# Performance work log

Hardware: AMD Instinct MI355X
Metric: run time of the kernel (lower is better)

The kernel has to match this reference:

```python
import jax, jax.numpy as jnp
import numpy as np

N = 4096      # num_nodes
U = 64        # num_units
IN = 2        # input_dim
DIM = U + IN  # 66
H = 4         # attention heads
ALPHA = 0.2   # leaky slope inside attention scores
SLOPE = 0.01  # nn.LeakyReLU() default for subnet activations
NEG_INF = -9e15


def setup_inputs() -> dict:
    key = jax.random.key(0)
    ks = jax.random.split(key, 20)
    def gn(k, shape, fan):
        return jax.random.normal(k, shape, dtype=jnp.float32) / np.float32(np.sqrt(fan))
    adj = jax.random.randint(ks[2], (N, N), 0, 2, dtype=jnp.int32)
    adj = jnp.maximum(adj, jnp.eye(N, dtype=jnp.int32))  # ensure self-loops
    return {
        "inputs": jax.random.normal(ks[0], (1, N * IN), dtype=jnp.float32),
        "hx": jax.random.normal(ks[1], (1, N, U), dtype=jnp.float32),
        "adj": adj,
        "m1_W": gn(ks[3], (H, DIM, DIM), DIM),
        "m1_a1": gn(ks[4], (H, DIM), DIM),
        "m1_a2": gn(ks[5], (H, DIM), DIM),
        "m1_Wout": gn(ks[6], (H * DIM, DIM), H * DIM),
        "m1_ao1": gn(ks[7], (DIM,), DIM),
        "m1_ao2": gn(ks[8], (DIM,), DIM),
        "m2_W": gn(ks[9], (H, DIM, DIM), DIM),
        "m2_a1": gn(ks[10], (H, DIM), DIM),
        "m2_a2": gn(ks[11], (H, DIM), DIM),
        "m2_Wout": gn(ks[12], (H * DIM, DIM), H * DIM),
        "m2_ao1": gn(ks[13], (DIM,), DIM),
        "m2_ao2": gn(ks[14], (DIM,), DIM),
        "g1_W": gn(ks[15], (DIM, 2 * U), DIM),
        "g1_b": jnp.zeros((2 * U,), dtype=jnp.float32),
        "g2_W": gn(ks[16], (DIM, U), DIM),
        "g2_b": jnp.zeros((U,), dtype=jnp.float32),
    }


def gat_layer(x, W, a1, a2, mask):
    # x: [N,Fin], W: [Fin,Fout], a1/a2: [Fout], mask: [N,N] bool
    h = x @ W                                   # [N,Fout]
    f1 = h @ a1                                 # [N] source term
    f2 = h @ a2                                 # [N] target term
    e = jax.nn.leaky_relu(f1[:, None] + f2[None, :], ALPHA)  # [N,N]
    e = jnp.where(mask, e, NEG_INF)
    attn = jax.nn.softmax(e, axis=-1)
    return attn @ h                             # [N,Fout]


def subnet(x, W, a1, a2, Wout, ao1, ao2, mask):
    # multi-head GAT, concat heads, activation, output GAT layer, activation
    heads = jax.vmap(gat_layer, in_axes=(None, 0, 0, 0, None))(x, W, a1, a2, mask)  # [H,N,DIM]
    hcat = jnp.transpose(heads, (1, 0, 2)).reshape(x.shape[0], -1)                   # [N,H*DIM]
    hcat = jax.nn.leaky_relu(hcat, SLOPE)
    out = gat_layer(hcat, Wout, ao1, ao2, mask)                                      # [N,DIM]
    return jax.nn.leaky_relu(out, SLOPE)


def reference(inputs, hx, adj, m1_W, m1_a1, m1_a2, m1_Wout, m1_ao1, m1_ao2,
              m2_W, m2_a1, m2_a2, m2_Wout, m2_ao1, m2_ao2,
              g1_W, g1_b, g2_W, g2_b):
    mask = adj > 0
    xi = inputs.reshape(N, IN)
    xh = hx.reshape(N, U)
    # _GAT1: concat(inputs, hx) -> GATSubNet1 -> linear -> sigmoid -> split r,u
    x1 = jnp.concatenate([xi, xh], axis=-1)                 # [N,DIM]
    g1 = subnet(x1, m1_W, m1_a1, m1_a2, m1_Wout, m1_ao1, m1_ao2, mask)
    value = jax.nn.sigmoid(g1 @ g1_W + g1_b)                # [N,2U]
    r, u = value[:, :U], value[:, U:]
    # _GAT2: concat(inputs, r*hx) -> GATSubNet2 -> linear -> tanh
    x2 = jnp.concatenate([xi, r * xh], axis=-1)             # [N,DIM]
    g2 = subnet(x2, m2_W, m2_a1, m2_a2, m2_Wout, m2_ao1, m2_ao2, mask)
    c = jnp.tanh(g2 @ g2_W + g2_b)                          # [N,U]
    new_state = u * xh + (1.0 - u) * c
    return new_state.reshape(1, N, U)
```

## Files before the change

### kernel.cpp

```cpp
#include <hip/hip_runtime.h>

constexpr int kN = 4096;
constexpr int kDim = 66;
constexpr int kU = 64;
constexpr float kAlpha = 0.2f;
constexpr float kSlope = 0.01f;
constexpr float kLog2e = 1.44269504f;

typedef _Float16 half8 __attribute__((ext_vector_type(8)));
typedef _Float16 half2t __attribute__((ext_vector_type(2)));
typedef float floatx4 __attribute__((ext_vector_type(4)));

__device__ inline unsigned int fkey(float f){
  unsigned int u = __float_as_uint(f);
  return (u & 0x80000000u) ? ~u : (u | 0x80000000u);
}
__device__ inline float funkey(unsigned int k){
  unsigned int u = (k & 0x80000000u) ? (k ^ 0x80000000u) : ~k;
  return __uint_as_float(u);
}

__global__ void setup_k(const int* __restrict__ adj, unsigned long long* __restrict__ packed,
                        const float* __restrict__ in2, const float* __restrict__ hx,
                        _Float16* __restrict__ x1b, _Float16* __restrict__ x2b,
                        const float* __restrict__ m1W, const float* __restrict__ m1a1, const float* __restrict__ m1a2,
                        const float* __restrict__ m1Wo, const float* __restrict__ m1ao1, const float* __restrict__ m1ao2,
                        const float* __restrict__ m2W, const float* __restrict__ m2a1, const float* __restrict__ m2a2,
                        const float* __restrict__ m2Wo, const float* __restrict__ m2ao1, const float* __restrict__ m2ao2,
                        const float* __restrict__ g1W, const float* __restrict__ g1b,
                        const float* __restrict__ g2W, const float* __restrict__ g2b,
                        _Float16* __restrict__ B1t, _Float16* __restrict__ B1t2,
                        _Float16* __restrict__ B2t, _Float16* __restrict__ B2t2,
                        _Float16* __restrict__ Bgt, _Float16* __restrict__ Bft,
                        unsigned int* __restrict__ fmaxbuf){
  int bb = blockIdx.x, t = threadIdx.x;
  if (bb < 16384){
    int gid = bb * 256 + t;
    unsigned long long m = __ballot(adj[gid] != 0);
    if ((t & 63) == 0) packed[gid >> 6] = m;
    return;
  }
  if (bb < 16384 + 1024){
    int i = (bb - 16384) * 4 + (t >> 6);
    int c = t & 63;
    x1b[(size_t)i * 96 + 2 + c] = (_Float16)hx[(size_t)i * kU + c];
    if (c < 2){
      _Float16 xv = (_Float16)in2[i * 2 + c];
      x1b[(size_t)i * 96 + c] = xv;
      x2b[(size_t)i * 96 + c] = xv;
    }
    if (c < 30){
      x1b[(size_t)i * 96 + 66 + c] = (_Float16)0.f;
      x2b[(size_t)i * 96 + 66 + c] = (_Float16)0.f;
    }
    return;
  }
  int b = bb - (16384 + 1024);
  if (b < 8){
    int m = b & 3;
    const float* W  = (b < 4 ? m1W  : m2W)  + (size_t)m * kDim * kDim;
    const float* a1 = (b < 4 ? m1a1 : m2a1) + m * kDim;
    const float* a2 = (b < 4 ? m1a2 : m2a2) + m * kDim;
    _Float16* Bo = (b < 4 ? B1t : B1t2) + (size_t)m * 80 * 96;
    __shared__ float Ws[kDim * kDim];
    __shared__ float wa1s[kDim], wa2s[kDim];
    for (int z = t; z < kDim * kDim; z += 256) Ws[z] = W[z];
    __syncthreads();
    if (t < kDim){
      float s1 = 0.f, s2 = 0.f;
      for (int d = 0; d < kDim; d++){ float wv = Ws[t * kDim + d]; s1 += wv * a1[d]; s2 += wv * a2[d]; }
      wa1s[t] = s1; wa2s[t] = s2;
    }
    __syncthreads();
    for (int z = t; z < 80 * 96; z += 256){
      int nn = z / 96, k = z % 96;
      float val = 0.f;
      if (k < kDim){
        if (nn < kDim) val = Ws[k * kDim + nn];
        else if (nn == 66) val = wa1s[k];
        else if (nn == 67) val = wa2s[k];
      }
      Bo[z] = (_Float16)val;
    }
  } else if (b < 10){
    const float* Wo  = (b == 8 ? m1Wo  : m2Wo);
    const float* ao1 = (b == 8 ? m1ao1 : m2ao1);
    const float* ao2 = (b == 8 ? m1ao2 : m2ao2);
    _Float16* Bo = (b == 8 ? B2t : B2t2);
    __shared__ float wo1s[264], wo2s[264];
    for (int k = t; k < 264; k += 256){
      float s1 = 0.f, s2 = 0.f;
      for (int d = 0; d < kDim; d++){ float wv = Wo[(size_t)k * kDim + d]; s1 += wv * ao1[d]; s2 += wv * ao2[d]; }
      wo1s[k] = s1; wo2s[k] = s2;
    }
    __syncthreads();
    for (int z = t; z < 80 * 288; z += 256){
      int nn = z / 288, k = z % 288;
      float val = 0.f;
      if (k < 264){
        if (nn < kDim) val = Wo[(size_t)k * kDim + nn];
        else if (nn == 66) val = wo1s[k];
        else if (nn == 67) val = wo2s[k];
      }
      Bo[z] = (_Float16)val;
    }
  } else if (b == 10){
    for (int z = t; z < 128 * 96; z += 256){
      int nn = z / 96, k = z % 96;
      float val = 0.f;
      if (k < kDim) val = g1W[k * 128 + nn];
      else if (k == 66) val = g1b[nn];
      Bgt[z] = (_Float16)val;
    }
  } else {
    if (t < 16) fmaxbuf[t] = 0u;
    for (int z = t; z < 64 * 96; z += 256){
      int nn = z / 96, k = z % 96;
      float val = 0.f;
      if (k < kDim) val = g2W[k * 64 + nn];
      else if (k == 66) val = g2b[nn];
      Bft[z] = (_Float16)val;
    }
  }
}

template<int KSTEPS, int NT>
__device__ __forceinline__ void gemmN(const _Float16* __restrict__ Arow,
                                      const _Float16* __restrict__ Bt, floatx4* acc){
  const int lane = threadIdx.x & 63, q = lane >> 4, n = lane & 15;
  #pragma unroll
  for (int v = 0; v < NT; v++) acc[v] = (floatx4){0.f, 0.f, 0.f, 0.f};
  #pragma unroll
  for (int ks = 0; ks < KSTEPS; ks++){
    half8 af = *(const half8*)&Arow[ks * 32 + q * 8];
    #pragma unroll
    for (int nt = 0; nt < NT; nt++){
      half8 bf = *(const half8*)&Bt[(size_t)(nt * 16 + n) * (KSTEPS * 32) + ks * 32 + q * 8];
      acc[nt] = __builtin_amdgcn_mfma_f32_16x16x32_f16(af, bf, acc[nt], 0, 0, 0);
    }
  }
}

__device__ __forceinline__ void epi0(floatx4* acc, int i0, _Float16* __restrict__ Htc,
                                     float* __restrict__ f1c, float* __restrict__ f2c,
                                     unsigned* __restrict__ fmaxslot){
  const int t = threadIdx.x, w = t >> 6, lane = t & 63, q = lane >> 4, n = lane & 15;
  const int ib = i0 + w * 16 + q * 4;
  float lm = -3e38f;
  #pragma unroll
  for (int nt = 0; nt < 5; nt++){
    int c = nt * 16 + n;
    if (c < kDim){
      union { _Float16 h[4]; uint2 v; } pk;
      pk.h[0] = (_Float16)acc[nt][0]; pk.h[1] = (_Float16)acc[nt][1];
      pk.h[2] = (_Float16)acc[nt][2]; pk.h[3] = (_Float16)acc[nt][3];
      *(uint2*)&Htc[(size_t)c * kN + ib] = pk.v;
    } else if (c == 66){
      float4 fv; fv.x = acc[nt][0] * kLog2e; fv.y = acc[nt][1] * kLog2e;
      fv.z = acc[nt][2] * kLog2e; fv.w = acc[nt][3] * kLog2e;
      *(float4*)&f1c[ib] = fv;
      *(uint2*)&Htc[(size_t)66 * kN + ib] = make_uint2(0x3C003C00u, 0x3C003C00u);
    } else if (c == 67){
      float4 fv; fv.x = acc[nt][0] * kLog2e; fv.y = acc[nt][1] * kLog2e;
      fv.z = acc[nt][2] * kLog2e; fv.w = acc[nt][3] * kLog2e;
      *(float4*)&f2c[ib] = fv;
      lm = fmaxf(fmaxf(fv.x, fv.y), fmaxf(fv.z, fv.w));
      *(uint2*)&Htc[(size_t)67 * kN + ib] = make_uint2(0u, 0u);
    }
  }
  lm = fmaxf(lm, __shfl_xor(lm, 16));
  lm = fmaxf(lm, __shfl_xor(lm, 32));
  if (lane == 3) atomicMax(fmaxslot, fkey(lm));
}

__global__ __launch_bounds__(256) void gemm_ht_k(
    const _Float16* __restrict__ A, const _Float16* __restrict__ Bt,
    _Float16* __restrict__ Ht, float* __restrict__ f1, float* __restrict__ f2,
    unsigned int* __restrict__ fmaxp)
{
  const int m = blockIdx.y;
  const int i0 = blockIdx.x * 64;
  const int w = threadIdx.x >> 6, n = threadIdx.x & 15;
  floatx4 acc[5];
  gemmN<3, 5>(A + (size_t)(i0 + w * 16 + n) * 96, Bt + (size_t)m * 80 * 96, acc);
  epi0(acc, i0, Ht + (size_t)m * 80 * kN, f1 + (size_t)m * kN, f2 + (size_t)m * kN, fmaxp + m);
}

template<int TPW, int KSR>
__global__ __launch_bounds__(256, 2) void attn_mfma_k(
    const _Float16* __restrict__ Ht, const float* __restrict__ f1,
    const float* __restrict__ f2, const unsigned int* __restrict__ fmaxu,
    const unsigned long long* __restrict__ packed,
    _Float16* __restrict__ paccb)
{
  constexpr int WJ = KSR * 32;
  const int m = blockIdx.y;
  const int t = threadIdx.x;
  const int w = t >> 6, lane = t & 63, q = lane >> 4, n = lane & 15;
  const int i0b = blockIdx.x * (TPW * 64);
  const int wrb = i0b + w * (TPW * 16);
  const int jbase = blockIdx.z * WJ;
  const _Float16* Hg = Ht + (size_t)m * 80 * kN;
  const float* f2m = f2 + (size_t)m * kN;
  const float* f1m = f1 + (size_t)m * kN;
  const float fmx = funkey(fmaxu[m]);

  __shared__ __align__(16) _Float16 B1h[WJ], B2h[WJ];
  for (int z = t; z < WJ; z += 256){
    float v = f2m[jbase + z] - fmx;
    B1h[z] = (_Float16)__builtin_amdgcn_exp2f(v);
    B2h[z] = (_Float16)__builtin_amdgcn_exp2f(kAlpha * v);
  }
  __syncthreads();

  half2t a1p[TPW], a2p[TPW];
  const unsigned long long* prow[TPW];
  #pragma unroll
  for (int a = 0; a < TPW; a++){
    int i = wrb + a * 16 + n;
    float t0 = f1m[i] + fmx;
    float S = fmaxf(t0, kAlpha * t0);
    _Float16 A1 = (_Float16)__builtin_amdgcn_exp2f(t0 - S);
    _Float16 A2 = (_Float16)__builtin_amdgcn_exp2f(kAlpha * t0 - S);
    a1p[a] = (half2t){A1, A1};
    a2p[a] = (half2t){A2, A2};
    prow[a] = packed + (size_t)i * 64;
  }

  floatx4 acc[TPW][5];
  #pragma unroll
  for (int a = 0; a < TPW; a++)
    #pragma unroll
    for (int v = 0; v < 5; v++) acc[a][v] = (floatx4){0.f, 0.f, 0.f, 0.f};

  unsigned long long mw[TPW];
  #pragma unroll
  for (int ks = 0; ks < KSR; ks++){
    if ((ks & 1) == 0){
      int widx = (jbase >> 6) + (ks >> 1);
      #pragma unroll
      for (int a = 0; a < TPW; a++) mw[a] = prow[a][widx];
    }
    const unsigned shift = (ks & 1) * 32 + q * 8;
    const int jo = ks * 32 + q * 8;
    union { uint4 v; unsigned u[4]; } b1v, b2v;
    b1v.v = *(const uint4*)&B1h[jo];
    b2v.v = *(const uint4*)&B2h[jo];
    union { half8 s; unsigned u[4]; } af[TPW];
    #pragma unroll
    for (int a = 0; a < TPW; a++){
      unsigned bits = (unsigned)((mw[a] >> shift) & 0xffull);
      #pragma unroll
      for (int e = 0; e < 4; e++){
        half2t x1 = __builtin_bit_cast(half2t, b1v.u[e]);
        half2t x2 = __builtin_bit_cast(half2t, b2v.u[e]);
        half2t pm = __builtin_elementwise_max(x1 * a1p[a], x2 * a2p[a]);
        unsigned mmk = (((bits >> (2 * e)) & 1u) ? 0x0000FFFFu : 0u)
                     | (((bits >> (2 * e + 1)) & 1u) ? 0xFFFF0000u : 0u);
        af[a].u[e] = __builtin_bit_cast(unsigned, pm) & mmk;
      }
    }
    const _Float16* hb = Hg + jbase + jo;
    #pragma unroll
    for (int nt = 0; nt < 5; nt++){
      half8 bf = *(const half8*)&hb[(size_t)(nt * 16 + n) * kN];
      #pragma unroll
      for (int a = 0; a < TPW; a++)
        acc[a][nt] = __builtin_amdgcn_mfma_f32_16x16x32_f16(af[a].s, bf, acc[a][nt], 0, 0, 0);
    }
  }
  const int slice = blockIdx.y * gridDim.z + blockIdx.z;
  _Float16* pw = paccb + ((size_t)slice * kN + wrb) * 72;
  #pragma unroll
  for (int a = 0; a < TPW; a++){
    #pragma unroll
    for (int nt = 0; nt < 5; nt++){
      if (nt < 4 || n < 4){
        #pragma unroll
        for (int r = 0; r < 4; r++)
          pw[(a * 16 + q * 4 + r) * 72 + nt * 16 + n] = (_Float16)acc[a][nt][r];
      }
    }
  }
}

__global__ __launch_bounds__(256) void combineH_gemmO_k(
    const _Float16* __restrict__ pacc, const _Float16* __restrict__ B2tc,
    _Float16* __restrict__ Htoc, float* __restrict__ fo1c, float* __restrict__ fo2c,
    unsigned int* __restrict__ fmaxslot)
{
  __shared__ __align__(16) _Float16 hcatL[64 * 296];
  const int t = threadIdx.x;
  const int i0 = blockIdx.x * 64;
  {
    const int mm = t >> 6, row = t & 63;
    const _Float16* pb = pacc + ((size_t)(mm * 8) * kN + (i0 + row)) * 72;
    constexpr size_t jstep = (size_t)kN * 72;
    float l = 0.f;
    #pragma unroll
    for (int s = 0; s < 8; s++) l += (float)pb[s * jstep + 66];
    float inv = 1.f / l;
    _Float16* hr = hcatL + row * 296 + mm * 66;
    #pragma unroll
    for (int c8 = 0; c8 < 9; c8++){
      float sv[8] = {0.f,0.f,0.f,0.f,0.f,0.f,0.f,0.f};
      #pragma unroll
      for (int s = 0; s < 8; s++){
        half8 hv = *(const half8*)&pb[s * jstep + c8 * 8];
        #pragma unroll
        for (int e = 0; e < 8; e++) sv[e] += (float)hv[e];
      }
      #pragma unroll
      for (int e = 0; e < 8; e++){
        int c = c8 * 8 + e;
        if (c < kDim){
          float vv = sv[e] * inv;
          vv = fmaxf(vv, kSlope * vv);
          hr[c] = (_Float16)vv;
        }
      }
    }
  }
  for (int z = t; z < 64 * 32; z += 256)
    hcatL[(z >> 5) * 296 + 264 + (z & 31)] = (_Float16)0.f;
  __syncthreads();
  const int w = t >> 6, n = t & 15;
  floatx4 acc[5];
  gemmN<9, 5>(hcatL + (w * 16 + n) * 296, B2tc, acc);
  epi0(acc, i0, Htoc, fo1c, fo2c, fmaxslot);
}

template<int EPI>
__global__ __launch_bounds__(256) void combineO_gemm_k(
    const _Float16* __restrict__ pacc, const _Float16* __restrict__ Btc,
    float* __restrict__ uv, const float* __restrict__ hxp,
    _Float16* __restrict__ x2bp, float* __restrict__ outp)
{
  __shared__ __align__(16) _Float16 gbL[64 * 104];
  __shared__ float lds_l[64];
  const int t = threadIdx.x;
  const int i0 = blockIdx.x * 64;
  {
    const int row = t >> 2, part = t & 3;
    const _Float16* pb = pacc + (size_t)(i0 + row) * 72;
    constexpr size_t jstep = (size_t)kN * 72;
    const int nt_tiles = (part == 0) ? 3 : 2;
    int tiles[3] = { part, part + 4, 8 };
    float sums[3][8];
    #pragma unroll
    for (int ti = 0; ti < 3; ti++)
      #pragma unroll
      for (int e = 0; e < 8; e++) sums[ti][e] = 0.f;
    for (int s = 0; s < 16; s++){
      for (int ti = 0; ti < nt_tiles; ti++){
        half8 hv = *(const half8*)&pb[s * jstep + tiles[ti] * 8];
        #pragma unroll
        for (int e = 0; e < 8; e++) sums[ti][e] += (float)hv[e];
      }
    }
    if (part == 0) lds_l[row] = sums[2][2];
    __syncthreads();
    float inv = 1.f / lds_l[row];
    _Float16* gr = gbL + row * 104;
    for (int ti = 0; ti < nt_tiles; ti++){
      int T = tiles[ti];
      #pragma unroll
      for (int e = 0; e < 8; e++){
        int c = T * 8 + e;
        if (c < kDim){
          float vv = sums[ti][e] * inv;
          vv = fmaxf(vv, kSlope * vv);
          gr[c] = (_Float16)vv;
        } else if (c == 66) gr[66] = (_Float16)1.f;
        else if (c == 67) gr[67] = (_Float16)0.f;
      }
    }
    #pragma unroll
    for (int e = 0; e < 9; e++) gr[68 + part * 9 + e] = (_Float16)0.f;
  }
  __syncthreads();
  const int w = t >> 6, lane = t & 63, q = lane >> 4, n = lane & 15;
  const int ib = i0 + w * 16 + q * 4;
  if constexpr (EPI == 1){
    floatx4 acc[8];
    gemmN<3, 8>(gbL + (w * 16 + n) * 104, Btc, acc);
    #pragma unroll
    for (int nt = 0; nt < 8; nt++){
      int c = nt * 16 + n;
      #pragma unroll
      for (int r = 0; r < 4; r++){
        float v = 1.f / (1.f + __expf(-acc[nt][r]));
        if (c < 64) x2bp[(size_t)(ib + r) * 96 + 2 + c] = (_Float16)(v * hxp[(size_t)(ib + r) * kU + c]);
        else        uv[(size_t)(ib + r) * kU + (c - 64)] = v;
      }
    }
  } else {
    floatx4 acc[4];
    gemmN<3, 4>(gbL + (w * 16 + n) * 104, Btc, acc);
    #pragma unroll
    for (int nt = 0; nt < 4; nt++){
      int c = nt * 16 + n;
      #pragma unroll
      for (int r = 0; r < 4; r++){
        float cc2 = tanhf(acc[nt][r]);
        float u2 = uv[(size_t)(ib + r) * kU + c];
        outp[(size_t)(ib + r) * kU + c] = u2 * hxp[(size_t)(ib + r) * kU + c] + (1.f - u2) * cc2;
      }
    }
  }
}

extern "C" void kernel_launch(void* const* d_in, const int* in_sizes, int n_in,
                              void* d_out, int out_size, void* d_ws, size_t ws_size,
                              hipStream_t stream){
  const float* inputs  = (const float*)d_in[0];
  const float* hx      = (const float*)d_in[1];
  const int*   adj     = (const int*)d_in[2];
  const float* m1_W    = (const float*)d_in[3];
  const float* m1_a1   = (const float*)d_in[4];
  const float* m1_a2   = (const float*)d_in[5];
  const float* m1_Wout = (const float*)d_in[6];
  const float* m1_ao1  = (const float*)d_in[7];
  const float* m1_ao2  = (const float*)d_in[8];
  const float* m2_W    = (const float*)d_in[9];
  const float* m2_a1   = (const float*)d_in[10];
  const float* m2_a2   = (const float*)d_in[11];
  const float* m2_Wout = (const float*)d_in[12];
  const float* m2_ao1  = (const float*)d_in[13];
  const float* m2_ao2  = (const float*)d_in[14];
  const float* g1_W    = (const float*)d_in[15];
  const float* g1_b    = (const float*)d_in[16];
  const float* g2_W    = (const float*)d_in[17];
  const float* g2_b    = (const float*)d_in[18];
  float* out = (float*)d_out;

  char* ws = (char*)d_ws;
  size_t off = 0;
  auto alloc = [&](size_t bytes) -> void* {
    void* p = ws + off;
    off = (off + bytes + 255) & ~(size_t)255;
    return p;
  };
  unsigned long long* packed = (unsigned long long*)alloc((size_t)kN * 64 * 8);
  _Float16* x1b  = (_Float16*)alloc((size_t)kN * 96 * 2);
  _Float16* x2b  = (_Float16*)alloc((size_t)kN * 96 * 2);
  _Float16* Ht   = (_Float16*)alloc((size_t)4 * 80 * kN * 2);
  _Float16* Hto  = (_Float16*)alloc((size_t)80 * kN * 2);
  float* f1   = (float*)alloc((size_t)4 * kN * 4);
  float* f2   = (float*)alloc((size_t)4 * kN * 4);
  float* fo1  = (float*)alloc((size_t)kN * 4);
  float* fo2  = (float*)alloc((size_t)kN * 4);
  unsigned int* fmaxbuf = (unsigned int*)alloc(64);
  float* u    = (float*)alloc((size_t)kN * kU * 4);
  _Float16* pacc = (_Float16*)alloc((size_t)32 * kN * 72 * 2);
  _Float16* B1t  = (_Float16*)alloc((size_t)4 * 80 * 96 * 2);
  _Float16* B1t2 = (_Float16*)alloc((size_t)4 * 80 * 96 * 2);
  _Float16* B2t  = (_Float16*)alloc((size_t)80 * 288 * 2);
  _Float16* B2t2 = (_Float16*)alloc((size_t)80 * 288 * 2);
  _Float16* Bgt  = (_Float16*)alloc((size_t)128 * 96 * 2);
  _Float16* Bft  = (_Float16*)alloc((size_t)64 * 96 * 2);
  (void)ws_size; (void)in_sizes; (void)n_in; (void)out_size;

  setup_k<<<16384 + 1024 + 12, 256, 0, stream>>>(adj, packed, inputs, hx, x1b, x2b,
      m1_W, m1_a1, m1_a2, m1_Wout, m1_ao1, m1_ao2,
      m2_W, m2_a1, m2_a2, m2_Wout, m2_ao1, m2_ao2,
      g1_W, g1_b, g2_W, g2_b,
      B1t, B1t2, B2t, B2t2, Bgt, Bft, fmaxbuf);

  gemm_ht_k<<<dim3(64, 4), 256, 0, stream>>>(x1b, B1t, Ht, f1, f2, fmaxbuf + 0);
  attn_mfma_k<4, 16><<<dim3(16, 4, 8), 256, 0, stream>>>(Ht, f1, f2, fmaxbuf + 0, packed, pacc);
  combineH_gemmO_k<<<64, 256, 0, stream>>>(pacc, B2t, Hto, fo1, fo2, fmaxbuf + 4);
  attn_mfma_k<2, 8><<<dim3(32, 1, 16), 256, 0, stream>>>(Hto, fo1, fo2, fmaxbuf + 4, packed, pacc);
  combineO_gemm_k<1><<<64, 256, 0, stream>>>(pacc, Bgt, u, hx, x2b, nullptr);

  gemm_ht_k<<<dim3(64, 4), 256, 0, stream>>>(x2b, B1t2, Ht, f1, f2, fmaxbuf + 5);
  attn_mfma_k<4, 16><<<dim3(16, 4, 8), 256, 0, stream>>>(Ht, f1, f2, fmaxbuf + 5, packed, pacc);
  combineH_gemmO_k<<<64, 256, 0, stream>>>(pacc, B2t2, Hto, fo1, fo2, fmaxbuf + 9);
  attn_mfma_k<2, 8><<<dim3(32, 1, 16), 256, 0, stream>>>(Hto, fo1, fo2, fmaxbuf + 9, packed, pacc);
  combineO_gemm_k<2><<<64, 256, 0, stream>>>(pacc, Bft, u, hx, nullptr, out);
}
```

Baseline: 364.6 us.

## Stage H tiles in LDS and loop over j-chunks inside attention blocks

The attention kernel now has each block walk a larger j-range in 128-column chunks. Each chunk's H tile and exp factors are staged in shared memory so the four waves share them instead of each reading H from global memory. For the head layer this cuts the number of partial slices from 8 to 4, which shrinks the pacc buffer and the combine work. The combineO reduction is also rewritten into a per-column scalar sum without the shared-memory row-sum sync. The trade-off is extra barriers per chunk, more LDS use per block, and less vectorized loads in combineO.

```diff
diff --git a/kernel.cpp b/kernel.cpp
--- a/kernel.cpp
+++ b/kernel.cpp
@@ -186,32 +186,24 @@
   epi0(acc, i0, Ht + (size_t)m * 80 * kN, f1 + (size_t)m * kN, f2 + (size_t)m * kN, fmaxp + m);
 }
 
-template<int TPW, int KSR>
+template<int TPW, int JSPLIT>
 __global__ __launch_bounds__(256, 2) void attn_mfma_k(
     const _Float16* __restrict__ Ht, const float* __restrict__ f1,
     const float* __restrict__ f2, const unsigned int* __restrict__ fmaxu,
     const unsigned long long* __restrict__ packed,
     _Float16* __restrict__ paccb)
 {
-  constexpr int WJ = KSR * 32;
-  const int m = blockIdx.y;
+  constexpr int JR = kN / JSPLIT;
+  constexpr int NCH = JR / 128;
+  const int m = blockIdx.y, js = blockIdx.z;
+  const int i0b = blockIdx.x * (TPW * 64);
   const int t = threadIdx.x;
   const int w = t >> 6, lane = t & 63, q = lane >> 4, n = lane & 15;
-  const int i0b = blockIdx.x * (TPW * 64);
   const int wrb = i0b + w * (TPW * 16);
-  const int jbase = blockIdx.z * WJ;
   const _Float16* Hg = Ht + (size_t)m * 80 * kN;
   const float* f2m = f2 + (size_t)m * kN;
   const float* f1m = f1 + (size_t)m * kN;
   const float fmx = funkey(fmaxu[m]);
-
-  __shared__ __align__(16) _Float16 B1h[WJ], B2h[WJ];
-  for (int z = t; z < WJ; z += 256){
-    float v = f2m[jbase + z] - fmx;
-    B1h[z] = (_Float16)__builtin_amdgcn_exp2f(v);
-    B2h[z] = (_Float16)__builtin_amdgcn_exp2f(kAlpha * v);
-  }
-  __syncthreads();
 
   half2t a1p[TPW], a2p[TPW];
   const unsigned long long* prow[TPW];
@@ -227,50 +219,67 @@
     prow[a] = packed + (size_t)i * 64;
   }
 
+  __shared__ __align__(16) _Float16 HtL[80 * 136];
+  __shared__ __align__(16) _Float16 B1h[128], B2h[128];
+  for (int z = t; z < 12 * 136; z += 256) HtL[68 * 136 + z] = (_Float16)0.f;
+
   floatx4 acc[TPW][5];
   #pragma unroll
   for (int a = 0; a < TPW; a++)
     #pragma unroll
     for (int v = 0; v < 5; v++) acc[a][v] = (floatx4){0.f, 0.f, 0.f, 0.f};
 
-  unsigned long long mw[TPW];
-  #pragma unroll
-  for (int ks = 0; ks < KSR; ks++){
-    if ((ks & 1) == 0){
-      int widx = (jbase >> 6) + (ks >> 1);
-      #pragma unroll
-      for (int a = 0; a < TPW; a++) mw[a] = prow[a][widx];
-    }
-    const unsigned shift = (ks & 1) * 32 + q * 8;
-    const int jo = ks * 32 + q * 8;
-    union { uint4 v; unsigned u[4]; } b1v, b2v;
-    b1v.v = *(const uint4*)&B1h[jo];
-    b2v.v = *(const uint4*)&B2h[jo];
-    union { half8 s; unsigned u[4]; } af[TPW];
+  const int jbase = js * JR;
+  for (int ch = 0; ch < NCH; ch++){
+    const int j0 = jbase + ch * 128;
+    __syncthreads();
+    for (int z = t; z < 68 * 16; z += 256){
+      int row = z >> 4, c16 = z & 15;
+      *(uint4*)&HtL[row * 136 + c16 * 8] = *(const uint4*)&Hg[(size_t)row * kN + j0 + c16 * 8];
+    }
+    if (t < 128){
+      float v = f2m[j0 + t] - fmx;
+      B1h[t] = (_Float16)__builtin_amdgcn_exp2f(v);
+      B2h[t] = (_Float16)__builtin_amdgcn_exp2f(kAlpha * v);
+    }
+    __syncthreads();
+    unsigned long long mw0[TPW], mw1[TPW];
     #pragma unroll
     for (int a = 0; a < TPW; a++){
-      unsigned bits = (unsigned)((mw[a] >> shift) & 0xffull);
-      #pragma unroll
-      for (int e = 0; e < 4; e++){
-        half2t x1 = __builtin_bit_cast(half2t, b1v.u[e]);
-        half2t x2 = __builtin_bit_cast(half2t, b2v.u[e]);
-        half2t pm = __builtin_elementwise_max(x1 * a1p[a], x2 * a2p[a]);
-        unsigned mmk = (((bits >> (2 * e)) & 1u) ? 0x0000FFFFu : 0u)
-                     | (((bits >> (2 * e + 1)) & 1u) ? 0xFFFF0000u : 0u);
-        af[a].u[e] = __builtin_bit_cast(unsigned, pm) & mmk;
-      }
-    }
-    const _Float16* hb = Hg + jbase + jo;
-    #pragma unroll
-    for (int nt = 0; nt < 5; nt++){
-      half8 bf = *(const half8*)&hb[(size_t)(nt * 16 + n) * kN];
-      #pragma unroll
-      for (int a = 0; a < TPW; a++)
-        acc[a][nt] = __builtin_amdgcn_mfma_f32_16x16x32_f16(af[a].s, bf, acc[a][nt], 0, 0, 0);
-    }
-  }
-  const int slice = blockIdx.y * gridDim.z + blockIdx.z;
-  _Float16* pw = paccb + ((size_t)slice * kN + wrb) * 72;
+      mw0[a] = prow[a][(j0 >> 6)];
+      mw1[a] = prow[a][(j0 >> 6) + 1];
+    }
+    #pragma unroll
+    for (int ks = 0; ks < 4; ks++){
+      const unsigned shift = (ks & 1) * 32 + q * 8;
+      const int jo = ks * 32 + q * 8;
+      union { uint4 v; unsigned u[4]; } b1v, b2v;
+      b1v.v = *(const uint4*)&B1h[jo];
+      b2v.v = *(const uint4*)&B2h[jo];
+      union { half8 s; unsigned u[4]; } af[TPW];
+      #pragma unroll
+      for (int a = 0; a < TPW; a++){
+        unsigned bits = (unsigned)(((ks < 2 ? mw0[a] : mw1[a]) >> shift) & 0xffull);
+        #pragma unroll
+        for (int e = 0; e < 4; e++){
+          half2t x1 = __builtin_bit_cast(half2t, b1v.u[e]);
+          half2t x2 = __builtin_bit_cast(half2t, b2v.u[e]);
+          half2t pm = __builtin_elementwise_max(x1 * a1p[a], x2 * a2p[a]);
+          unsigned mmk = (((bits >> (2 * e)) & 1u) ? 0x0000FFFFu : 0u)
+                       | (((bits >> (2 * e + 1)) & 1u) ? 0xFFFF0000u : 0u);
+          af[a].u[e] = __builtin_bit_cast(unsigned, pm) & mmk;
+        }
+      }
+      #pragma unroll
+      for (int nt = 0; nt < 5; nt++){
+        const half8 bf = *(const half8*)&HtL[(nt * 16 + n) * 136 + jo];
+        #pragma unroll
+        for (int a = 0; a < TPW; a++)
+          acc[a][nt] = __builtin_amdgcn_mfma_f32_16x16x32_f16(af[a].s, bf, acc[a][nt], 0, 0, 0);
+      }
+    }
+  }
+  _Float16* pw = paccb + ((size_t)(m * JSPLIT + js) * kN + wrb) * 72;
   #pragma unroll
   for (int a = 0; a < TPW; a++){
     #pragma unroll
@@ -294,18 +303,18 @@
   const int i0 = blockIdx.x * 64;
   {
     const int mm = t >> 6, row = t & 63;
-    const _Float16* pb = pacc + ((size_t)(mm * 8) * kN + (i0 + row)) * 72;
+    const _Float16* pb = pacc + ((size_t)(mm * 4) * kN + (i0 + row)) * 72;
     constexpr size_t jstep = (size_t)kN * 72;
     float l = 0.f;
     #pragma unroll
-    for (int s = 0; s < 8; s++) l += (float)pb[s * jstep + 66];
+    for (int s = 0; s < 4; s++) l += (float)pb[s * jstep + 66];
     float inv = 1.f / l;
     _Float16* hr = hcatL + row * 296 + mm * 66;
     #pragma unroll
     for (int c8 = 0; c8 < 9; c8++){
       float sv[8] = {0.f,0.f,0.f,0.f,0.f,0.f,0.f,0.f};
       #pragma unroll
-      for (int s = 0; s < 8; s++){
+      for (int s = 0; s < 4; s++){
         half8 hv = *(const half8*)&pb[s * jstep + c8 * 8];
         #pragma unroll
         for (int e = 0; e < 8; e++) sv[e] += (float)hv[e];
@@ -337,46 +346,30 @@
     _Float16* __restrict__ x2bp, float* __restrict__ outp)
 {
   __shared__ __align__(16) _Float16 gbL[64 * 104];
-  __shared__ float lds_l[64];
   const int t = threadIdx.x;
   const int i0 = blockIdx.x * 64;
   {
-    const int row = t >> 2, part = t & 3;
+    const int row = t >> 2, cg = t & 3;
     const _Float16* pb = pacc + (size_t)(i0 + row) * 72;
     constexpr size_t jstep = (size_t)kN * 72;
-    const int nt_tiles = (part == 0) ? 3 : 2;
-    int tiles[3] = { part, part + 4, 8 };
-    float sums[3][8];
-    #pragma unroll
-    for (int ti = 0; ti < 3; ti++)
-      #pragma unroll
-      for (int e = 0; e < 8; e++) sums[ti][e] = 0.f;
-    for (int s = 0; s < 16; s++){
-      for (int ti = 0; ti < nt_tiles; ti++){
-        half8 hv = *(const half8*)&pb[s * jstep + tiles[ti] * 8];
+    float l = 0.f;
+    #pragma unroll
+    for (int s = 0; s < 16; s++) l += (float)pb[s * jstep + 66];
+    float inv = 1.f / l;
+    _Float16* gr = gbL + row * 104;
+    for (int cc = 0; cc < 17; cc++){
+      int c = cg * 17 + cc;
+      if (c < kDim){
+        float vv = 0.f;
         #pragma unroll
-        for (int e = 0; e < 8; e++) sums[ti][e] += (float)hv[e];
-      }
-    }
-    if (part == 0) lds_l[row] = sums[2][2];
-    __syncthreads();
-    float inv = 1.f / lds_l[row];
-    _Float16* gr = gbL + row * 104;
-    for (int ti = 0; ti < nt_tiles; ti++){
-      int T = tiles[ti];
-      #pragma unroll
-      for (int e = 0; e < 8; e++){
-        int c = T * 8 + e;
-        if (c < kDim){
-          float vv = sums[ti][e] * inv;
-          vv = fmaxf(vv, kSlope * vv);
-          gr[c] = (_Float16)vv;
-        } else if (c == 66) gr[66] = (_Float16)1.f;
-        else if (c == 67) gr[67] = (_Float16)0.f;
-      }
-    }
-    #pragma unroll
-    for (int e = 0; e < 9; e++) gr[68 + part * 9 + e] = (_Float16)0.f;
+        for (int s = 0; s < 16; s++) vv += (float)pb[s * jstep + c];
+        vv *= inv; vv = fmaxf(vv, kSlope * vv);
+        gr[c] = (_Float16)vv;
+      } else if (c == 66) gr[66] = (_Float16)1.f;
+      else if (c == 67) gr[67] = (_Float16)0.f;
+    }
+    #pragma unroll
+    for (int e = 0; e < 9; e++) gr[68 + cg * 9 + e] = (_Float16)0.f;
   }
   __syncthreads();
   const int w = t >> 6, lane = t & 63, q = lane >> 4, n = lane & 15;
@@ -452,7 +445,7 @@
   float* fo2  = (float*)alloc((size_t)kN * 4);
   unsigned int* fmaxbuf = (unsigned int*)alloc(64);
   float* u    = (float*)alloc((size_t)kN * kU * 4);
-  _Float16* pacc = (_Float16*)alloc((size_t)32 * kN * 72 * 2);
+  _Float16* pacc = (_Float16*)alloc((size_t)16 * kN * 72 * 2);
   _Float16* B1t  = (_Float16*)alloc((size_t)4 * 80 * 96 * 2);
   _Float16* B1t2 = (_Float16*)alloc((size_t)4 * 80 * 96 * 2);
   _Float16* B2t  = (_Float16*)alloc((size_t)80 * 288 * 2);
@@ -468,14 +461,14 @@
       B1t, B1t2, B2t, B2t2, Bgt, Bft, fmaxbuf);
 
   gemm_ht_k<<<dim3(64, 4), 256, 0, stream>>>(x1b, B1t, Ht, f1, f2, fmaxbuf + 0);
-  attn_mfma_k<4, 16><<<dim3(16, 4, 8), 256, 0, stream>>>(Ht, f1, f2, fmaxbuf + 0, packed, pacc);
+  attn_mfma_k<2, 4><<<dim3(32, 4, 4), 256, 0, stream>>>(Ht, f1, f2, fmaxbuf + 0, packed, pacc);
   combineH_gemmO_k<<<64, 256, 0, stream>>>(pacc, B2t, Hto, fo1, fo2, fmaxbuf + 4);
-  attn_mfma_k<2, 8><<<dim3(32, 1, 16), 256, 0, stream>>>(Hto, fo1, fo2, fmaxbuf + 4, packed, pacc);
+  attn_mfma_k<2, 16><<<dim3(32, 1, 16), 256, 0, stream>>>(Hto, fo1, fo2, fmaxbuf + 4, packed, pacc);
   combineO_gemm_k<1><<<64, 256, 0, stream>>>(pacc, Bgt, u, hx, x2b, nullptr);
 
   gemm_ht_k<<<dim3(64, 4), 256, 0, stream>>>(x2b, B1t2, Ht, f1, f2, fmaxbuf + 5);
-  attn_mfma_k<4, 16><<<dim3(16, 4, 8), 256, 0, stream>>>(Ht, f1, f2, fmaxbuf + 5, packed, pacc);
+  attn_mfma_k<2, 4><<<dim3(32, 4, 4), 256, 0, stream>>>(Ht, f1, f2, fmaxbuf + 5, packed, pacc);
   combineH_gemmO_k<<<64, 256, 0, stream>>>(pacc, B2t2, Hto, fo1, fo2, fmaxbuf + 9);
-  attn_mfma_k<2, 8><<<dim3(32, 1, 16), 256, 0, stream>>>(Hto, fo1, fo2, fmaxbuf + 9, packed, pacc);
+  attn_mfma_k<2, 16><<<dim3(32, 1, 16), 256, 0, stream>>>(Hto, fo1, fo2, fmaxbuf + 9, packed, pacc);
   combineO_gemm_k<2><<<64, 256, 0, stream>>>(pacc, Bft, u, hx, nullptr, out);
 }
```

Result: faster. 339.7 us (-6.8%).
